# Optimization experiments

Hardware: AMD Instinct MI355X
Metric: run time of the kernel (lower is better)

## Reference

```python
import jax, jax.numpy as jnp
import numpy as np

N = 50000      # nodes
E = 800000     # directed edges (before self loops)
F_IN = 2613    # raw feature dim (nn.Linear(2613, 256))
D = 256        # hidden dim, heads = 1
BN_EPS = 1e-5
NEG_SLOPE = 0.2  # PyG GATConv default negative_slope


def setup_inputs() -> dict:
    key = jax.random.key(0)
    ks = jax.random.split(key, 12)

    def glorot(k, shape):
        s = (6.0 / (shape[0] + shape[-1])) ** 0.5
        return jax.random.uniform(k, shape, jnp.float32, -s, s)

    zeros = lambda: jnp.zeros((D,), jnp.float32)
    ones = lambda: jnp.ones((D,), jnp.float32)
    return {
        "x": jax.random.normal(ks[0], (N, F_IN), dtype=jnp.float32),
        "edges": jax.random.randint(ks[1], (2, E), 0, N, dtype=jnp.int32),
        "W1": glorot(ks[2], (F_IN, D)), "b1": zeros(),
        "W2": glorot(ks[3], (D, D)), "b2": zeros(),
        "W3": glorot(ks[4], (D, D)), "b3": zeros(),
        "g1": ones(), "be1": zeros(),
        "g2": ones(), "be2": zeros(),
        "g3": ones(), "be3": zeros(),
        "Wg1": glorot(ks[5], (D, D)),
        "att_src1": glorot(ks[6], (D,)), "att_dst1": glorot(ks[7], (D,)),
        "bg1": zeros(), "g4": ones(), "be4": zeros(),
        "Wg2": glorot(ks[8], (D, D)),
        "att_src2": glorot(ks[9], (D,)), "att_dst2": glorot(ks[10], (D,)),
        "bg2": zeros(), "g5": ones(), "be5": zeros(),
    }


def batch_norm(h, gamma, beta):
    # BatchNorm1d in training mode: batch statistics over the node axis
    mu = h.mean(axis=0)
    var = h.var(axis=0)
    return (h - mu) * jax.lax.rsqrt(var + BN_EPS) * gamma + beta


def gat_conv(h, W, att_src, att_dst, bias, src, dst):
    # PyG GATConv, heads=1: shared linear for src/dst, additive attention,
    # leaky_relu scores, softmax over incoming edges per destination node.
    xl = h @ W                              # [N, D]
    a_src = xl @ att_src                    # [N]
    a_dst = xl @ att_dst                    # [N]
    e = jax.nn.leaky_relu(a_src[src] + a_dst[dst], NEG_SLOPE)  # [E+N]
    m = jax.ops.segment_max(jax.lax.stop_gradient(e), dst, num_segments=N)
    w = jnp.exp(e - m[dst])
    denom = jax.ops.segment_sum(w, dst, num_segments=N)
    alpha = w / (denom[dst] + 1e-16)        # [E+N]
    out = jax.ops.segment_sum(alpha[:, None] * xl[src], dst, num_segments=N)
    return out + bias


def reference(x, edges, W1, b1, W2, b2, W3, b3, g1, be1, g2, be2, g3, be3,
              Wg1, att_src1, att_dst1, bg1, g4, be4,
              Wg2, att_src2, att_dst2, bg2, g5, be5):
    # PyG GATConv default add_self_loops=True
    loops = jnp.arange(N, dtype=edges.dtype)
    src = jnp.concatenate([edges[0], loops])
    dst = jnp.concatenate([edges[1], loops])

    h = jax.nn.elu(batch_norm(x @ W1 + b1, g1, be1))
    h = jax.nn.elu(batch_norm(h @ W2 + b2, g2, be2))
    h = jax.nn.elu(batch_norm(h @ W3 + b3, g3, be3))
    h = gat_conv(h, Wg1, att_src1, att_dst1, bg1, src, dst)
    h = jax.nn.elu(batch_norm(h, g4, be4))
    h = gat_conv(h, Wg2, att_src2, att_dst2, bg2, src, dst)
    h = jax.nn.elu(batch_norm(h, g5, be5))
    return h
```

## Files before the change

### kernel.cpp

```cpp
#include <hip/hip_runtime.h>

#define DEV __device__ __forceinline__

typedef __attribute__((ext_vector_type(4))) float f32x4;
typedef __attribute__((ext_vector_type(8))) short short8;

DEV float bf2f(unsigned short u) {
    union { unsigned int i; float f; } c;
    c.i = ((unsigned int)u) << 16;
    return c.f;
}
DEV unsigned short f2bf(float f) {
    union { float f; unsigned int i; } c;
    c.f = f;
    unsigned int u = c.i;
    u += 0x7FFFu + ((u >> 16) & 1u);
    return (unsigned short)(u >> 16);
}

__global__ void cvt_pad_k(const float* __restrict__ x, unsigned short* __restrict__ xb,
                          int M, int K, int Kp) {
    const int gpr = Kp >> 3;
    const long long total = (long long)M * gpr;
    for (long long g = blockIdx.x * (long long)blockDim.x + threadIdx.x; g < total;
         g += (long long)gridDim.x * blockDim.x) {
        const int row = (int)(g / gpr);
        const int c8  = (int)(g - (long long)row * gpr);
        const int k0  = c8 * 8;
        const float* src = x + (size_t)row * K + k0;
        unsigned int w[4];
        if (k0 + 8 <= K) {
            f32x4 v0 = *(const f32x4*)(src);
            f32x4 v1 = *(const f32x4*)(src + 4);
            w[0] = (unsigned int)f2bf(v0[0]) | ((unsigned int)f2bf(v0[1]) << 16);
            w[1] = (unsigned int)f2bf(v0[2]) | ((unsigned int)f2bf(v0[3]) << 16);
            w[2] = (unsigned int)f2bf(v1[0]) | ((unsigned int)f2bf(v1[1]) << 16);
            w[3] = (unsigned int)f2bf(v1[2]) | ((unsigned int)f2bf(v1[3]) << 16);
        } else {
            unsigned short o[8];
            #pragma unroll
            for (int j = 0; j < 8; ++j) o[j] = (k0 + j < K) ? f2bf(src[j]) : (unsigned short)0;
            w[0] = o[0] | ((unsigned int)o[1] << 16);
            w[1] = o[2] | ((unsigned int)o[3] << 16);
            w[2] = o[4] | ((unsigned int)o[5] << 16);
            w[3] = o[6] | ((unsigned int)o[7] << 16);
        }
        *(uint4*)(xb + (size_t)row * Kp + k0) = *(uint4*)w;
    }
}

template<bool OUT_BF16, bool STATS>
__launch_bounds__(512)
__global__ void gemm_k(const unsigned short* __restrict__ A,
                       const unsigned short* __restrict__ Bt,
                       void* __restrict__ Cptr,
                       float* __restrict__ st,
                       int M, int lda, int ldb, int ksteps)
{
    __shared__ __align__(16) unsigned short As[2][128 * 64];
    __shared__ __align__(16) unsigned short Bs[2][256 * 64];
    const int t    = threadIdx.x;
    const int wid  = t >> 6;
    const int lane = t & 63;
    const int wr   = wid >> 2;
    const int wc   = wid & 3;
    const int m0   = blockIdx.x * 128;

    f32x4 acc[4][4] = {};

    auto stageB = [&](int buf, int ks) {
        const int k0 = ks * 64;
        #pragma unroll
        for (int is = 0; is < 4; ++is) {
            const int rbase = wid * 32 + is * 8;
            const int rr  = rbase + (lane >> 3);
            const int csw = (lane & 7) ^ (rr & 7);
            __builtin_amdgcn_global_load_lds(
                (const __attribute__((address_space(1))) void*)(Bt + (size_t)rr * ldb + k0 + csw * 8),
                (__attribute__((address_space(3))) void*)(&Bs[buf][rbase * 64]),
                16, 0, 0);
        }
    };
    auto stageA = [&](int buf, int ks) {
        const int k0 = ks * 64;
        #pragma unroll
        for (int is = 0; is < 2; ++is) {
            const int rbase = wid * 16 + is * 8;
            const int rr  = rbase + (lane >> 3);
            const int csw = (lane & 7) ^ (rr & 7);
            __builtin_amdgcn_global_load_lds(
                (const __attribute__((address_space(1))) void*)(A + (size_t)(m0 + rr) * lda + k0 + csw * 8),
                (__attribute__((address_space(3))) void*)(&As[buf][rbase * 64]),
                16, 0, 0);
        }
    };
    auto compute = [&](int buf) {
        #pragma unroll
        for (int kk = 0; kk < 2; ++kk) {
            short8 af[4], bfr[4];
            #pragma unroll
            for (int mi = 0; mi < 4; ++mi) {
                const int r   = wr * 64 + mi * 16 + (lane & 15);
                const int csw = (kk * 4 + (lane >> 4)) ^ (r & 7);
                af[mi] = *(const short8*)(&As[buf][r * 64 + csw * 8]);
            }
            #pragma unroll
            for (int ni = 0; ni < 4; ++ni) {
                const int r   = wc * 64 + ni * 16 + (lane & 15);
                const int csw = (kk * 4 + (lane >> 4)) ^ (r & 7);
                bfr[ni] = *(const short8*)(&Bs[buf][r * 64 + csw * 8]);
            }
            #pragma unroll
            for (int mi = 0; mi < 4; ++mi)
                #pragma unroll
                for (int ni = 0; ni < 4; ++ni)
                    acc[mi][ni] = __builtin_amdgcn_mfma_f32_16x16x32_bf16(
                        af[mi], bfr[ni], acc[mi][ni], 0, 0, 0);
        }
    };

    stageA(0, 0); stageB(0, 0);
    __builtin_amdgcn_sched_barrier(0);
    stageA(1, 1); stageB(1, 1);
    asm volatile("s_waitcnt vmcnt(6)" ::: "memory");
    __builtin_amdgcn_sched_barrier(0);
    __builtin_amdgcn_s_barrier();
    __builtin_amdgcn_sched_barrier(0);

    int cur = 0;
    for (int k = 0; k < ksteps; ++k) {
        compute(cur);
        if (k + 1 >= ksteps) break;
        __builtin_amdgcn_sched_barrier(0);
        __builtin_amdgcn_s_barrier();
        __builtin_amdgcn_sched_barrier(0);
        if (k + 2 < ksteps) {
            stageA(cur, k + 2);
            stageB(cur, k + 2);
            asm volatile("s_waitcnt vmcnt(6)" ::: "memory");
        } else {
            asm volatile("s_waitcnt vmcnt(0)" ::: "memory");
        }
        __builtin_amdgcn_sched_barrier(0);
        __builtin_amdgcn_s_barrier();
        __builtin_amdgcn_sched_barrier(0);
        cur ^= 1;
    }

    #pragma unroll
    for (int mi = 0; mi < 4; ++mi) {
        #pragma unroll
        for (int ni = 0; ni < 4; ++ni) {
            const int col = wc * 64 + ni * 16 + (lane & 15);
            #pragma unroll
            for (int rg = 0; rg < 4; ++rg) {
                const int m = m0 + wr * 64 + mi * 16 + (lane >> 4) * 4 + rg;
                if (m < M) {
                    if constexpr (OUT_BF16)
                        ((unsigned short*)Cptr)[(size_t)m * 256 + col] = f2bf(acc[mi][ni][rg]);
                    else
                        ((float*)Cptr)[(size_t)m * 256 + col] = acc[mi][ni][rg];
                }
            }
        }
    }
    if constexpr (STATS) {
        #pragma unroll
        for (int ni = 0; ni < 4; ++ni) {
            float s = 0.f, q = 0.f;
            #pragma unroll
            for (int mi = 0; mi < 4; ++mi)
                #pragma unroll
                for (int rg = 0; rg < 4; ++rg) {
                    const int m = m0 + wr * 64 + mi * 16 + (lane >> 4) * 4 + rg;
                    const float v = (m < M) ? acc[mi][ni][rg] : 0.f;
                    s += v; q += v * v;
                }
            s += __shfl_xor(s, 16); q += __shfl_xor(q, 16);
            s += __shfl_xor(s, 32); q += __shfl_xor(q, 32);
            if (lane < 16) {
                const int col = wc * 64 + ni * 16 + lane;
                atomicAdd(&st[col], s);
                atomicAdd(&st[256 + col], q);
            }
        }
    }
}

__global__ void wtrans_k(const float* __restrict__ W, unsigned short* __restrict__ WT,
                         int K, int ldb) {
    int total = 256 * ldb;
    for (int idx = blockIdx.x * blockDim.x + threadIdx.x; idx < total;
         idx += gridDim.x * blockDim.x) {
        int n = idx / ldb, k = idx - n * ldb;
        WT[idx] = f2bf(k < K ? W[(size_t)k * 256 + n] : 0.f);
    }
}

__global__ void colstats_k(const float* __restrict__ h, float* st, int total4) {
    const int gid    = blockIdx.x * 256 + threadIdx.x;
    const int stride = gridDim.x * 256;
    float4 s = {0.f, 0.f, 0.f, 0.f}, q = {0.f, 0.f, 0.f, 0.f};
    for (int i = gid; i < total4; i += stride) {
        float4 v = ((const float4*)h)[i];
        s.x += v.x; s.y += v.y; s.z += v.z; s.w += v.w;
        q.x += v.x * v.x; q.y += v.y * v.y; q.z += v.z * v.z; q.w += v.w * v.w;
    }
    __shared__ float red[2][4][64][4];
    const int wid = threadIdx.x >> 6, lane = threadIdx.x & 63;
    *(float4*)&red[0][wid][lane][0] = s;
    *(float4*)&red[1][wid][lane][0] = q;
    __syncthreads();
    if (wid == 0) {
        float4 s0 = *(float4*)&red[0][0][lane][0];
        float4 q0 = *(float4*)&red[1][0][lane][0];
        #pragma unroll
        for (int w = 1; w < 4; ++w) {
            float4 sw = *(float4*)&red[0][w][lane][0];
            float4 qw = *(float4*)&red[1][w][lane][0];
            s0.x += sw.x; s0.y += sw.y; s0.z += sw.z; s0.w += sw.w;
            q0.x += qw.x; q0.y += qw.y; q0.z += qw.z; q0.w += qw.w;
        }
        atomicAdd(&st[lane * 4 + 0], s0.x);
        atomicAdd(&st[lane * 4 + 1], s0.y);
        atomicAdd(&st[lane * 4 + 2], s0.z);
        atomicAdd(&st[lane * 4 + 3], s0.w);
        atomicAdd(&st[256 + lane * 4 + 0], q0.x);
        atomicAdd(&st[256 + lane * 4 + 1], q0.y);
        atomicAdd(&st[256 + lane * 4 + 2], q0.z);
        atomicAdd(&st[256 + lane * 4 + 3], q0.w);
    }
}

__global__ void bnfinal_k(const float* __restrict__ st, const float* __restrict__ g,
                          const float* __restrict__ be, float* __restrict__ ss, float invN) {
    int c = threadIdx.x;
    float mu  = st[c] * invN;
    float var = st[256 + c] * invN - mu * mu;
    float sc  = g[c] * rsqrtf(var + 1e-5f);
    ss[c]       = sc;
    ss[256 + c] = be[c] - mu * sc;
}

template<bool OUT_BF16>
__global__ void bnelu_k(const float* h, const float* ss, void* outp, int total4) {
    for (int i = blockIdx.x * blockDim.x + threadIdx.x; i < total4;
         i += gridDim.x * blockDim.x) {
        float4 v = ((const float4*)h)[i];
        int c = (i << 2) & 255;
        float4 y;
        y.x = fmaf(v.x, ss[c + 0], ss[256 + c + 0]);
        y.y = fmaf(v.y, ss[c + 1], ss[256 + c + 1]);
        y.z = fmaf(v.z, ss[c + 2], ss[256 + c + 2]);
        y.w = fmaf(v.w, ss[c + 3], ss[256 + c + 3]);
        y.x = y.x > 0.f ? y.x : expm1f(y.x);
        y.y = y.y > 0.f ? y.y : expm1f(y.y);
        y.z = y.z > 0.f ? y.z : expm1f(y.z);
        y.w = y.w > 0.f ? y.w : expm1f(y.w);
        if (OUT_BF16) {
            ushort4 o;
            o.x = f2bf(y.x); o.y = f2bf(y.y); o.z = f2bf(y.z); o.w = f2bf(y.w);
            ((ushort4*)outp)[i] = o;
        } else {
            ((float4*)outp)[i] = y;
        }
    }
}

__global__ void adot_k(const unsigned short* __restrict__ xl, const float* __restrict__ as_,
                       const float* __restrict__ ad_, float* __restrict__ a_src,
                       float* __restrict__ a_dst, int N) {
    int w = (blockIdx.x * blockDim.x + threadIdx.x) >> 6;
    int lane = threadIdx.x & 63;
    if (w >= N) return;
    ushort4 v = *(const ushort4*)(xl + (size_t)w * 256 + lane * 4);
    float4 s4 = *(const float4*)(as_ + lane * 4);
    float4 d4 = *(const float4*)(ad_ + lane * 4);
    float x0 = bf2f(v.x), x1 = bf2f(v.y), x2 = bf2f(v.z), x3 = bf2f(v.w);
    float ps = x0 * s4.x + x1 * s4.y + x2 * s4.z + x3 * s4.w;
    float pd = x0 * d4.x + x1 * d4.y + x2 * d4.z + x3 * d4.w;
    #pragma unroll
    for (int off = 32; off; off >>= 1) {
        ps += __shfl_xor(ps, off);
        pd += __shfl_xor(pd, off);
    }
    if (lane == 0) { a_src[w] = ps; a_dst[w] = pd; }
}

DEV float lrelu(float e) { return e > 0.f ? e : 0.2f * e; }

__global__ void gat_k(const unsigned short* __restrict__ xl, const float* __restrict__ a_src,
                      const float* __restrict__ a_dst, const int* __restrict__ csr,
                      const int* __restrict__ indptr, float* __restrict__ out, int N) {
    int d = (blockIdx.x * blockDim.x + threadIdx.x) >> 6;
    int lane = threadIdx.x & 63;
    if (d >= N) return;
    int beg = indptr[d], end = indptr[d + 1];
    float adst = a_dst[d];
    float mx = -1e30f;
    for (int i = beg + lane; i < end; i += 64)
        mx = fmaxf(mx, lrelu(a_src[csr[i]] + adst));
    #pragma unroll
    for (int off = 32; off; off >>= 1) mx = fmaxf(mx, __shfl_xor(mx, off));
    float sm = 0.f;
    for (int i = beg + lane; i < end; i += 64)
        sm += __expf(lrelu(a_src[csr[i]] + adst) - mx);
    #pragma unroll
    for (int off = 32; off; off >>= 1) sm += __shfl_xor(sm, off);
    float inv = 1.f / (sm + 1e-16f);

    float4 A0 = {0,0,0,0}, A1 = {0,0,0,0}, A2 = {0,0,0,0}, A3 = {0,0,0,0};
    int i = beg;
    for (; i + 4 <= end; i += 4) {
        int s0 = csr[i], s1 = csr[i+1], s2 = csr[i+2], s3 = csr[i+3];
        float w0 = __expf(lrelu(a_src[s0] + adst) - mx) * inv;
        float w1 = __expf(lrelu(a_src[s1] + adst) - mx) * inv;
        float w2 = __expf(lrelu(a_src[s2] + adst) - mx) * inv;
        float w3 = __expf(lrelu(a_src[s3] + adst) - mx) * inv;
        ushort4 v0 = *(const ushort4*)(xl + (size_t)s0 * 256 + lane * 4);
        ushort4 v1 = *(const ushort4*)(xl + (size_t)s1 * 256 + lane * 4);
        ushort4 v2 = *(const ushort4*)(xl + (size_t)s2 * 256 + lane * 4);
        ushort4 v3 = *(const ushort4*)(xl + (size_t)s3 * 256 + lane * 4);
        A0.x += w0 * bf2f(v0.x); A0.y += w0 * bf2f(v0.y); A0.z += w0 * bf2f(v0.z); A0.w += w0 * bf2f(v0.w);
        A1.x += w1 * bf2f(v1.x); A1.y += w1 * bf2f(v1.y); A1.z += w1 * bf2f(v1.z); A1.w += w1 * bf2f(v1.w);
        A2.x += w2 * bf2f(v2.x); A2.y += w2 * bf2f(v2.y); A2.z += w2 * bf2f(v2.z); A2.w += w2 * bf2f(v2.w);
        A3.x += w3 * bf2f(v3.x); A3.y += w3 * bf2f(v3.y); A3.z += w3 * bf2f(v3.z); A3.w += w3 * bf2f(v3.w);
    }
    for (; i < end; ++i) {
        int s = csr[i];
        float w = __expf(lrelu(a_src[s] + adst) - mx) * inv;
        ushort4 v = *(const ushort4*)(xl + (size_t)s * 256 + lane * 4);
        A0.x += w * bf2f(v.x); A0.y += w * bf2f(v.y);
        A0.z += w * bf2f(v.z); A0.w += w * bf2f(v.w);
    }
    A0.x += A1.x + A2.x + A3.x;
    A0.y += A1.y + A2.y + A3.y;
    A0.z += A1.z + A2.z + A3.z;
    A0.w += A1.w + A2.w + A3.w;
    *(float4*)(out + (size_t)d * 256 + lane * 4) = A0;
}

__global__ void hist_k(const int* __restrict__ edges, int* deg, int E, int N) {
    int total = E + N;
    for (int i = blockIdx.x * blockDim.x + threadIdx.x; i < total;
         i += gridDim.x * blockDim.x) {
        int dd = (i < E) ? edges[E + i] : (i - E);
        atomicAdd(&deg[dd], 1);
    }
}

__global__ void scan1_k(const int* __restrict__ deg, int* iscan, int* bsum, int N) {
    int i = blockIdx.x * 256 + threadIdx.x;
    int lane = threadIdx.x & 63, wid = threadIdx.x >> 6;
    int v = (i < N) ? deg[i] : 0;
    #pragma unroll
    for (int off = 1; off < 64; off <<= 1) {
        int u = __shfl_up(v, off);
        if (lane >= off) v += u;
    }
    __shared__ int wsum[4];
    if (lane == 63) wsum[wid] = v;
    __syncthreads();
    #pragma unroll
    for (int w = 0; w < 3; ++w) if (wid > w) v += wsum[w];
    if (i < N) iscan[i] = v;
    if (threadIdx.x == 255) bsum[blockIdx.x] = v;
}

__global__ void scan2_k(int* bsum, int nb) {
    int t = threadIdx.x;
    int lane = t & 63, wid = t >> 6;
    int v = (t < nb) ? bsum[t] : 0;
    int orig = v;
    #pragma unroll
    for (int off = 1; off < 64; off <<= 1) {
        int u = __shfl_up(v, off);
        if (lane >= off) v += u;
    }
    __shared__ int wsum[4];
    if (lane == 63) wsum[wid] = v;
    __syncthreads();
    #pragma unroll
    for (int w = 0; w < 3; ++w) if (wid > w) v += wsum[w];
    if (t < nb) bsum[t] = v - orig;
}

__global__ void scan3_k(const int* __restrict__ iscan, const int* __restrict__ boff,
                        int* indptr, int N) {
    int i = blockIdx.x * 256 + threadIdx.x;
    if (i < N) indptr[i + 1] = iscan[i] + boff[blockIdx.x];
    if (i == 0) indptr[0] = 0;
}

__global__ void copy_k(const int* __restrict__ a, int* b, int N) {
    for (int i = blockIdx.x * blockDim.x + threadIdx.x; i < N;
         i += gridDim.x * blockDim.x) b[i] = a[i];
}

__global__ void scatter_k(const int* __restrict__ edges, int* pos, int* csr, int E, int N) {
    int total = E + N;
    for (int i = blockIdx.x * blockDim.x + threadIdx.x; i < total;
         i += gridDim.x * blockDim.x) {
        int s  = (i < E) ? edges[i]     : (i - E);
        int dd = (i < E) ? edges[E + i] : (i - E);
        int slot = atomicAdd(&pos[dd], 1);
        csr[slot] = s;
    }
}

extern "C" void kernel_launch(void* const* d_in, const int* in_sizes, int n_in,
                              void* d_out, int out_size, void* d_ws, size_t ws_size,
                              hipStream_t stream) {
    const float* x     = (const float*)d_in[0];
    const int*   edges = (const int*)d_in[1];
    const float* W1 = (const float*)d_in[2];
    const float* W2 = (const float*)d_in[4];
    const float* W3 = (const float*)d_in[6];
    const float* g1 = (const float*)d_in[8],  *be1 = (const float*)d_in[9];
    const float* g2 = (const float*)d_in[10], *be2 = (const float*)d_in[11];
    const float* g3 = (const float*)d_in[12], *be3 = (const float*)d_in[13];
    const float* Wg1 = (const float*)d_in[14];
    const float* as1 = (const float*)d_in[15], *ad1 = (const float*)d_in[16];
    const float* g4 = (const float*)d_in[18], *be4 = (const float*)d_in[19];
    const float* Wg2 = (const float*)d_in[20];
    const float* as2 = (const float*)d_in[21], *ad2 = (const float*)d_in[22];
    const float* g5 = (const float*)d_in[24], *be5 = (const float*)d_in[25];

    const int N    = out_size / 256;
    const int K1   = in_sizes[0] / N;
    const int E    = in_sizes[1] / 2;
    const int Etot = E + N;
    const int ks1  = (K1 + 63) / 64;
    const int ldb1 = ks1 * 64;

    char* p = (char*)d_ws;
    auto alloc = [&](size_t bytes) {
        char* r = p;
        p += (bytes + 255) & ~(size_t)255;
        return r;
    };
    unsigned short* W1T  = (unsigned short*)alloc((size_t)256 * ldb1 * 2);
    unsigned short* W2T  = (unsigned short*)alloc(256 * 256 * 2);
    unsigned short* W3T  = (unsigned short*)alloc(256 * 256 * 2);
    unsigned short* Wg1T = (unsigned short*)alloc(256 * 256 * 2);
    unsigned short* Wg2T = (unsigned short*)alloc(256 * 256 * 2);
    unsigned short* xb   = (unsigned short*)alloc((size_t)N * ldb1 * 2);
    unsigned short* hn   = (unsigned short*)alloc((size_t)N * 256 * 2);
    unsigned short* xl   = (unsigned short*)alloc((size_t)N * 256 * 2);
    float* a_src  = (float*)alloc((size_t)N * 4);
    float* a_dst  = (float*)alloc((size_t)N * 4);
    int*   deg    = (int*)alloc((size_t)N * 4);
    int*   iscan  = (int*)alloc((size_t)N * 4);
    int*   bsum   = (int*)alloc(1024);
    int*   indptr = (int*)alloc((size_t)(N + 1) * 4);
    int*   pos    = (int*)alloc((size_t)N * 4);
    int*   csr    = (int*)alloc((size_t)Etot * 4);
    float* st     = (float*)alloc(512 * 4);
    float* ss     = (float*)alloc(512 * 4);
    (void)alloc(1 << 19);
    float* out = (float*)d_out;

    const int nb = (N + 255) / 256;
    const int eg = (Etot + 255) / 256;
    const int gb = (N + 127) / 128;
    const int t4 = N * 64;
    const int bg4 = (t4 + 255) / 256;

    hipMemsetAsync(deg, 0, (size_t)N * 4, stream);
    hist_k<<<eg, 256, 0, stream>>>(edges, deg, E, N);
    scan1_k<<<nb, 256, 0, stream>>>(deg, iscan, bsum, N);
    scan2_k<<<1, 256, 0, stream>>>(bsum, nb);
    scan3_k<<<nb, 256, 0, stream>>>(iscan, bsum, indptr, N);
    copy_k<<<nb, 256, 0, stream>>>(indptr, pos, N);
    scatter_k<<<eg, 256, 0, stream>>>(edges, pos, csr, E, N);

    wtrans_k<<<(256 * ldb1 + 255) / 256, 256, 0, stream>>>(W1, W1T, K1, ldb1);
    wtrans_k<<<256, 256, 0, stream>>>(W2, W2T, 256, 256);
    wtrans_k<<<256, 256, 0, stream>>>(W3, W3T, 256, 256);
    wtrans_k<<<256, 256, 0, stream>>>(Wg1, Wg1T, 256, 256);
    wtrans_k<<<256, 256, 0, stream>>>(Wg2, Wg2T, 256, 256);
    cvt_pad_k<<<2048, 256, 0, stream>>>(x, xb, N, K1, ldb1);

    const float invN = 1.f / (float)N;

    hipMemsetAsync(st, 0, 2048, stream);
    gemm_k<false, true><<<gb, 512, 0, stream>>>(xb, W1T, out, st, N, ldb1, ldb1, ks1);
    bnfinal_k<<<1, 256, 0, stream>>>(st, g1, be1, ss, invN);
    bnelu_k<true><<<bg4, 256, 0, stream>>>(out, ss, hn, t4);

    hipMemsetAsync(st, 0, 2048, stream);
    gemm_k<false, true><<<gb, 512, 0, stream>>>(hn, W2T, out, st, N, 256, 256, 4);
    bnfinal_k<<<1, 256, 0, stream>>>(st, g2, be2, ss, invN);
    bnelu_k<true><<<bg4, 256, 0, stream>>>(out, ss, hn, t4);

    hipMemsetAsync(st, 0, 2048, stream);
    gemm_k<false, true><<<gb, 512, 0, stream>>>(hn, W3T, out, st, N, 256, 256, 4);
    bnfinal_k<<<1, 256, 0, stream>>>(st, g3, be3, ss, invN);
    bnelu_k<true><<<bg4, 256, 0, stream>>>(out, ss, hn, t4);

    gemm_k<true, false><<<gb, 512, 0, stream>>>(hn, Wg1T, xl, st, N, 256, 256, 4);
    adot_k<<<(N + 3) / 4, 256, 0, stream>>>(xl, as1, ad1, a_src, a_dst, N);
    gat_k<<<(N + 3) / 4, 256, 0, stream>>>(xl, a_src, a_dst, csr, indptr, out, N);
    hipMemsetAsync(st, 0, 2048, stream);
    colstats_k<<<1024, 256, 0, stream>>>(out, st, t4);
    bnfinal_k<<<1, 256, 0, stream>>>(st, g4, be4, ss, invN);
    bnelu_k<true><<<bg4, 256, 0, stream>>>(out, ss, hn, t4);

    gemm_k<true, false><<<gb, 512, 0, stream>>>(hn, Wg2T, xl, st, N, 256, 256, 4);
    adot_k<<<(N + 3) / 4, 256, 0, stream>>>(xl, as2, ad2, a_src, a_dst, N);
    gat_k<<<(N + 3) / 4, 256, 0, stream>>>(xl, a_src, a_dst, csr, indptr, out, N);
    hipMemsetAsync(st, 0, 2048, stream);
    colstats_k<<<1024, 256, 0, stream>>>(out, st, t4);
    bnfinal_k<<<1, 256, 0, stream>>>(st, g5, be5, ss, invN);
    bnelu_k<false><<<bg4, 256, 0, stream>>>(out, ss, out, t4);
}
```

Baseline: 998.3 us.

## Store intermediates in bf16, triple-buffer GEMM, fuse BN finalize, online softmax in GAT

Several separate changes. GEMM outputs and GAT outputs are now written as bf16 instead of fp32, roughly halving intermediate write and read traffic, and the bnfinal kernel is folded into bnelu, which now runs a fixed grid-stride launch. The GEMM moves from double to triple LDS buffering with deeper prefetch, and GAT merges its max and sum passes into one online-softmax pass. The costs are bf16 rounding before batch-norm statistics, which loses some accuracy, and three times the LDS footprint (147 KB), which may reduce occupancy.

```diff
diff --git a/kernel.cpp b/kernel.cpp
--- a/kernel.cpp
+++ b/kernel.cpp
@@ -49,16 +49,16 @@
     }
 }
 
-template<bool OUT_BF16, bool STATS>
+template<bool STATS>
 __launch_bounds__(512)
 __global__ void gemm_k(const unsigned short* __restrict__ A,
                        const unsigned short* __restrict__ Bt,
-                       void* __restrict__ Cptr,
+                       unsigned short* __restrict__ C,
                        float* __restrict__ st,
                        int M, int lda, int ldb, int ksteps)
 {
-    __shared__ __align__(16) unsigned short As[2][128 * 64];
-    __shared__ __align__(16) unsigned short Bs[2][256 * 64];
+    __shared__ __align__(16) unsigned short As[3][128 * 64];
+    __shared__ __align__(16) unsigned short Bs[3][256 * 64];
     const int t    = threadIdx.x;
     const int wid  = t >> 6;
     const int lane = t & 63;
@@ -68,20 +68,7 @@
 
     f32x4 acc[4][4] = {};
 
-    auto stageB = [&](int buf, int ks) {
-        const int k0 = ks * 64;
-        #pragma unroll
-        for (int is = 0; is < 4; ++is) {
-            const int rbase = wid * 32 + is * 8;
-            const int rr  = rbase + (lane >> 3);
-            const int csw = (lane & 7) ^ (rr & 7);
-            __builtin_amdgcn_global_load_lds(
-                (const __attribute__((address_space(1))) void*)(Bt + (size_t)rr * ldb + k0 + csw * 8),
-                (__attribute__((address_space(3))) void*)(&Bs[buf][rbase * 64]),
-                16, 0, 0);
-        }
-    };
-    auto stageA = [&](int buf, int ks) {
+    auto stage = [&](int buf, int ks) {
         const int k0 = ks * 64;
         #pragma unroll
         for (int is = 0; is < 2; ++is) {
@@ -91,6 +78,16 @@
             __builtin_amdgcn_global_load_lds(
                 (const __attribute__((address_space(1))) void*)(A + (size_t)(m0 + rr) * lda + k0 + csw * 8),
                 (__attribute__((address_space(3))) void*)(&As[buf][rbase * 64]),
+                16, 0, 0);
+        }
+        #pragma unroll
+        for (int is = 0; is < 4; ++is) {
+            const int rbase = wid * 32 + is * 8;
+            const int rr  = rbase + (lane >> 3);
+            const int csw = (lane & 7) ^ (rr & 7);
+            __builtin_amdgcn_global_load_lds(
+                (const __attribute__((address_space(1))) void*)(Bt + (size_t)rr * ldb + k0 + csw * 8),
+                (__attribute__((address_space(3))) void*)(&Bs[buf][rbase * 64]),
                 16, 0, 0);
         }
     };
@@ -119,10 +116,12 @@
         }
     };
 
-    stageA(0, 0); stageB(0, 0);
+    stage(0, 0);
     __builtin_amdgcn_sched_barrier(0);
-    stageA(1, 1); stageB(1, 1);
-    asm volatile("s_waitcnt vmcnt(6)" ::: "memory");
+    stage(1, 1);
+    __builtin_amdgcn_sched_barrier(0);
+    stage(2, 2);
+    asm volatile("s_waitcnt vmcnt(12)" ::: "memory");
     __builtin_amdgcn_sched_barrier(0);
     __builtin_amdgcn_s_barrier();
     __builtin_amdgcn_sched_barrier(0);
@@ -134,9 +133,10 @@
         __builtin_amdgcn_sched_barrier(0);
         __builtin_amdgcn_s_barrier();
         __builtin_amdgcn_sched_barrier(0);
-        if (k + 2 < ksteps) {
-            stageA(cur, k + 2);
-            stageB(cur, k + 2);
+        if (k + 3 < ksteps) {
+            stage(cur, k + 3);
+            asm volatile("s_waitcnt vmcnt(12)" ::: "memory");
+        } else if (k + 2 < ksteps) {
             asm volatile("s_waitcnt vmcnt(6)" ::: "memory");
         } else {
             asm volatile("s_waitcnt vmcnt(0)" ::: "memory");
@@ -144,7 +144,7 @@
         __builtin_amdgcn_sched_barrier(0);
         __builtin_amdgcn_s_barrier();
         __builtin_amdgcn_sched_barrier(0);
-        cur ^= 1;
+        cur = (cur == 2) ? 0 : cur + 1;
     }
 
     #pragma unroll
@@ -155,12 +155,8 @@
             #pragma unroll
             for (int rg = 0; rg < 4; ++rg) {
                 const int m = m0 + wr * 64 + mi * 16 + (lane >> 4) * 4 + rg;
-                if (m < M) {
-                    if constexpr (OUT_BF16)
-                        ((unsigned short*)Cptr)[(size_t)m * 256 + col] = f2bf(acc[mi][ni][rg]);
-                    else
-                        ((float*)Cptr)[(size_t)m * 256 + col] = acc[mi][ni][rg];
-                }
+                if (m < M)
+                    C[(size_t)m * 256 + col] = f2bf(acc[mi][ni][rg]);
             }
         }
     }
@@ -197,14 +193,15 @@
     }
 }
 
-__global__ void colstats_k(const float* __restrict__ h, float* st, int total4) {
+__global__ void colstats_k(const unsigned short* __restrict__ h, float* st, int total4) {
     const int gid    = blockIdx.x * 256 + threadIdx.x;
     const int stride = gridDim.x * 256;
     float4 s = {0.f, 0.f, 0.f, 0.f}, q = {0.f, 0.f, 0.f, 0.f};
     for (int i = gid; i < total4; i += stride) {
-        float4 v = ((const float4*)h)[i];
-        s.x += v.x; s.y += v.y; s.z += v.z; s.w += v.w;
-        q.x += v.x * v.x; q.y += v.y * v.y; q.z += v.z * v.z; q.w += v.w * v.w;
+        ushort4 v = ((const ushort4*)h)[i];
+        float x0 = bf2f(v.x), x1 = bf2f(v.y), x2 = bf2f(v.z), x3 = bf2f(v.w);
+        s.x += x0; s.y += x1; s.z += x2; s.w += x3;
+        q.x += x0 * x0; q.y += x1 * x1; q.z += x2 * x2; q.w += x3 * x3;
     }
     __shared__ float red[2][4][64][4];
     const int wid = threadIdx.x >> 6, lane = threadIdx.x & 63;
@@ -232,37 +229,40 @@
     }
 }
 
-__global__ void bnfinal_k(const float* __restrict__ st, const float* __restrict__ g,
-                          const float* __restrict__ be, float* __restrict__ ss, float invN) {
-    int c = threadIdx.x;
-    float mu  = st[c] * invN;
-    float var = st[256 + c] * invN - mu * mu;
-    float sc  = g[c] * rsqrtf(var + 1e-5f);
-    ss[c]       = sc;
-    ss[256 + c] = be[c] - mu * sc;
-}
-
-template<bool OUT_BF16>
-__global__ void bnelu_k(const float* h, const float* ss, void* outp, int total4) {
-    for (int i = blockIdx.x * blockDim.x + threadIdx.x; i < total4;
-         i += gridDim.x * blockDim.x) {
-        float4 v = ((const float4*)h)[i];
-        int c = (i << 2) & 255;
-        float4 y;
-        y.x = fmaf(v.x, ss[c + 0], ss[256 + c + 0]);
-        y.y = fmaf(v.y, ss[c + 1], ss[256 + c + 1]);
-        y.z = fmaf(v.z, ss[c + 2], ss[256 + c + 2]);
-        y.w = fmaf(v.w, ss[c + 3], ss[256 + c + 3]);
-        y.x = y.x > 0.f ? y.x : expm1f(y.x);
-        y.y = y.y > 0.f ? y.y : expm1f(y.y);
-        y.z = y.z > 0.f ? y.z : expm1f(y.z);
-        y.w = y.w > 0.f ? y.w : expm1f(y.w);
-        if (OUT_BF16) {
+template<bool OUT_F32>
+__global__ void bnelu_k(const unsigned short* __restrict__ h,
+                        const float* __restrict__ st, const float* __restrict__ g,
+                        const float* __restrict__ be, void* __restrict__ outp,
+                        int total4, float invN) {
+    const int gid    = blockIdx.x * 256 + threadIdx.x;
+    const int stride = gridDim.x * 256;
+    const int c      = (gid << 2) & 255;
+    float sc[4], sh[4];
+    #pragma unroll
+    for (int j = 0; j < 4; ++j) {
+        float mu  = st[c + j] * invN;
+        float var = st[256 + c + j] * invN - mu * mu;
+        float s   = g[c + j] * rsqrtf(var + 1e-5f);
+        sc[j] = s;
+        sh[j] = be[c + j] - mu * s;
+    }
+    for (int i = gid; i < total4; i += stride) {
+        ushort4 v = ((const ushort4*)h)[i];
+        float y0 = fmaf(bf2f(v.x), sc[0], sh[0]);
+        float y1 = fmaf(bf2f(v.y), sc[1], sh[1]);
+        float y2 = fmaf(bf2f(v.z), sc[2], sh[2]);
+        float y3 = fmaf(bf2f(v.w), sc[3], sh[3]);
+        y0 = y0 > 0.f ? y0 : expm1f(y0);
+        y1 = y1 > 0.f ? y1 : expm1f(y1);
+        y2 = y2 > 0.f ? y2 : expm1f(y2);
+        y3 = y3 > 0.f ? y3 : expm1f(y3);
+        if (OUT_F32) {
+            float4 o; o.x = y0; o.y = y1; o.z = y2; o.w = y3;
+            ((float4*)outp)[i] = o;
+        } else {
             ushort4 o;
-            o.x = f2bf(y.x); o.y = f2bf(y.y); o.z = f2bf(y.z); o.w = f2bf(y.w);
+            o.x = f2bf(y0); o.y = f2bf(y1); o.z = f2bf(y2); o.w = f2bf(y3);
             ((ushort4*)outp)[i] = o;
-        } else {
-            ((float4*)outp)[i] = y;
         }
     }
 }
@@ -291,23 +291,27 @@
 
 __global__ void gat_k(const unsigned short* __restrict__ xl, const float* __restrict__ a_src,
                       const float* __restrict__ a_dst, const int* __restrict__ csr,
-                      const int* __restrict__ indptr, float* __restrict__ out, int N) {
+                      const int* __restrict__ indptr, unsigned short* __restrict__ out, int N) {
     int d = (blockIdx.x * blockDim.x + threadIdx.x) >> 6;
     int lane = threadIdx.x & 63;
     if (d >= N) return;
     int beg = indptr[d], end = indptr[d + 1];
     float adst = a_dst[d];
-    float mx = -1e30f;
-    for (int i = beg + lane; i < end; i += 64)
-        mx = fmaxf(mx, lrelu(a_src[csr[i]] + adst));
+
+    float m = -1e30f, s = 0.f;
+    for (int i = beg + lane; i < end; i += 64) {
+        float e  = lrelu(a_src[csr[i]] + adst);
+        float nm = fmaxf(m, e);
+        s = s * __expf(m - nm) + __expf(e - nm);
+        m = nm;
+    }
+    float mx = m;
     #pragma unroll
     for (int off = 32; off; off >>= 1) mx = fmaxf(mx, __shfl_xor(mx, off));
-    float sm = 0.f;
-    for (int i = beg + lane; i < end; i += 64)
-        sm += __expf(lrelu(a_src[csr[i]] + adst) - mx);
-    #pragma unroll
-    for (int off = 32; off; off >>= 1) sm += __shfl_xor(sm, off);
-    float inv = 1.f / (sm + 1e-16f);
+    s *= __expf(m - mx);
+    #pragma unroll
+    for (int off = 32; off; off >>= 1) s += __shfl_xor(s, off);
+    float inv = 1.f / (s + 1e-16f);
 
     float4 A0 = {0,0,0,0}, A1 = {0,0,0,0}, A2 = {0,0,0,0}, A3 = {0,0,0,0};
     int i = beg;
@@ -327,17 +331,18 @@
         A3.x += w3 * bf2f(v3.x); A3.y += w3 * bf2f(v3.y); A3.z += w3 * bf2f(v3.z); A3.w += w3 * bf2f(v3.w);
     }
     for (; i < end; ++i) {
-        int s = csr[i];
-        float w = __expf(lrelu(a_src[s] + adst) - mx) * inv;
-        ushort4 v = *(const ushort4*)(xl + (size_t)s * 256 + lane * 4);
+        int sidx = csr[i];
+        float w = __expf(lrelu(a_src[sidx] + adst) - mx) * inv;
+        ushort4 v = *(const ushort4*)(xl + (size_t)sidx * 256 + lane * 4);
         A0.x += w * bf2f(v.x); A0.y += w * bf2f(v.y);
         A0.z += w * bf2f(v.z); A0.w += w * bf2f(v.w);
     }
-    A0.x += A1.x + A2.x + A3.x;
-    A0.y += A1.y + A2.y + A3.y;
-    A0.z += A1.z + A2.z + A3.z;
-    A0.w += A1.w + A2.w + A3.w;
-    *(float4*)(out + (size_t)d * 256 + lane * 4) = A0;
+    ushort4 o;
+    o.x = f2bf(A0.x + A1.x + A2.x + A3.x);
+    o.y = f2bf(A0.y + A1.y + A2.y + A3.y);
+    o.z = f2bf(A0.z + A1.z + A2.z + A3.z);
+    o.w = f2bf(A0.w + A1.w + A2.w + A3.w);
+    *(ushort4*)(out + (size_t)d * 256 + lane * 4) = o;
 }
 
 __global__ void hist_k(const int* __restrict__ edges, int* deg, int E, int N) {
@@ -445,7 +450,8 @@
     unsigned short* Wg1T = (unsigned short*)alloc(256 * 256 * 2);
     unsigned short* Wg2T = (unsigned short*)alloc(256 * 256 * 2);
     unsigned short* xb   = (unsigned short*)alloc((size_t)N * ldb1 * 2);
-    unsigned short* hn   = (unsigned short*)alloc((size_t)N * 256 * 2);
+    unsigned short* ha   = (unsigned short*)alloc((size_t)N * 256 * 2);
+    unsigned short* hb   = (unsigned short*)alloc((size_t)N * 256 * 2);
     unsigned short* xl   = (unsigned short*)alloc((size_t)N * 256 * 2);
     float* a_src  = (float*)alloc((size_t)N * 4);
     float* a_dst  = (float*)alloc((size_t)N * 4);
@@ -456,7 +462,6 @@
     int*   pos    = (int*)alloc((size_t)N * 4);
     int*   csr    = (int*)alloc((size_t)Etot * 4);
     float* st     = (float*)alloc(512 * 4);
-    float* ss     = (float*)alloc(512 * 4);
     (void)alloc(1 << 19);
     float* out = (float*)d_out;
 
@@ -464,7 +469,7 @@
     const int eg = (Etot + 255) / 256;
     const int gb = (N + 127) / 128;
     const int t4 = N * 64;
-    const int bg4 = (t4 + 255) / 256;
+    const float invN = 1.f / (float)N;
 
     hipMemsetAsync(deg, 0, (size_t)N * 4, stream);
     hist_k<<<eg, 256, 0, stream>>>(edges, deg, E, N);
@@ -481,36 +486,29 @@
     wtrans_k<<<256, 256, 0, stream>>>(Wg2, Wg2T, 256, 256);
     cvt_pad_k<<<2048, 256, 0, stream>>>(x, xb, N, K1, ldb1);
 
-    const float invN = 1.f / (float)N;
-
     hipMemsetAsync(st, 0, 2048, stream);
-    gemm_k<false, true><<<gb, 512, 0, stream>>>(xb, W1T, out, st, N, ldb1, ldb1, ks1);
-    bnfinal_k<<<1, 256, 0, stream>>>(st, g1, be1, ss, invN);
-    bnelu_k<true><<<bg4, 256, 0, stream>>>(out, ss, hn, t4);
+    gemm_k<true><<<gb, 512, 0, stream>>>(xb, W1T, ha, st, N, ldb1, ldb1, ks1);
+    bnelu_k<false><<<2048, 256, 0, stream>>>(ha, st, g1, be1, ha, t4, invN);
 
     hipMemsetAsync(st, 0, 2048, stream);
-    gemm_k<false, true><<<gb, 512, 0, stream>>>(hn, W2T, out, st, N, 256, 256, 4);
-    bnfinal_k<<<1, 256, 0, stream>>>(st, g2, be2, ss, invN);
-    bnelu_k<true><<<bg4, 256, 0, stream>>>(out, ss, hn, t4);
+    gemm_k<true><<<gb, 512, 0, stream>>>(ha, W2T, hb, st, N, 256, 256, 4);
+    bnelu_k<false><<<2048, 256, 0, stream>>>(hb, st, g2, be2, hb, t4, invN);
 
     hipMemsetAsync(st, 0, 2048, stream);
-    gemm_k<false, true><<<gb, 512, 0, stream>>>(hn, W3T, out, st, N, 256, 256, 4);
-    bnfinal_k<<<1, 256, 0, stream>>>(st, g3, be3, ss, invN);
-    bnelu_k<true><<<bg4, 256, 0, stream>>>(out, ss, hn, t4);
-
-    gemm_k<true, false><<<gb, 512, 0, stream>>>(hn, Wg1T, xl, st, N, 256, 256, 4);
+    gemm_k<true><<<gb, 512, 0, stream>>>(hb, W3T, ha, st, N, 256, 256, 4);
+    bnelu_k<false><<<2048, 256, 0, stream>>>(ha, st, g3, be3, ha, t4, invN);
+
+    gemm_k<false><<<gb, 512, 0, stream>>>(ha, Wg1T, xl, st, N, 256, 256, 4);
     adot_k<<<(N + 3) / 4, 256, 0, stream>>>(xl, as1, ad1, a_src, a_dst, N);
-    gat_k<<<(N + 3) / 4, 256, 0, stream>>>(xl, a_src, a_dst, csr, indptr, out, N);
+    gat_k<<<(N + 3) / 4, 256, 0, stream>>>(xl, a_src, a_dst, csr, indptr, hb, N);
     hipMemsetAsync(st, 0, 2048, stream);
-    colstats_k<<<1024, 256, 0, stream>>>(out, st, t4);
-    bnfinal_k<<<1, 256, 0, stream>>>(st, g4, be4, ss, invN);
-    bnelu_k<true><<<bg4, 256, 0, stream>>>(out, ss, hn, t4);
-
-    gemm_k<true, false><<<gb, 512, 0, stream>>>(hn, Wg2T, xl, st, N, 256, 256, 4);
+    colstats_k<<<1024, 256, 0, stream>>>(hb, st, t4);
+    bnelu_k<false><<<2048, 256, 0, stream>>>(hb, st, g4, be4, hb, t4, invN);
+
+    gemm_k<false><<<gb, 512, 0, stream>>>(hb, Wg2T, xl, st, N, 256, 256, 4);
     adot_k<<<(N + 3) / 4, 256, 0, stream>>>(xl, as2, ad2, a_src, a_dst, N);
-    gat_k<<<(N + 3) / 4, 256, 0, stream>>>(xl, a_src, a_dst, csr, indptr, out, N);
+    gat_k<<<(N + 3) / 4, 256, 0, stream>>>(xl, a_src, a_dst, csr, indptr, ha, N);
     hipMemsetAsync(st, 0, 2048, stream);
-    colstats_k<<<1024, 256, 0, stream>>>(out, st, t4);
-    bnfinal_k<<<1, 256, 0, stream>>>(st, g5, be5, ss, invN);
-    bnelu_k<false><<<bg4, 256, 0, stream>>>(out, ss, out, t4);
-}
+    colstats_k<<<1024, 256, 0, stream>>>(ha, st, t4);
+    bnelu_k<true><<<2048, 256, 0, stream>>>(ha, st, g5, be5, out, t4, invN);
+}
```

New measurement: 966.4 us. 1.03x faster.
